# Performance work log

Hardware: AMD Instinct MI355X
Metric: run time of the kernel (lower is better)

The kernel has to match this reference:

```python
import jax, jax.numpy as jnp
import numpy as np

B, L, F_OP, F_EU, D, H = 4, 512, 10, 2, 128, 128


def setup_inputs() -> dict:
    key = jax.random.key(0)
    ks = jax.random.split(key, 16)

    def lin_w(k, fin, fout):
        # kaiming-ish init, stored [in, out] so forward is x @ W + b
        return (jax.random.normal(k, (fin, fout), jnp.float32) * (1.0 / np.sqrt(fin)))

    return {
        "inputs": jax.random.normal(ks[0], (B, L, F_OP), jnp.float32),
        "coords": jax.random.normal(ks[1], (B, L, F_EU), jnp.float32),
        "targets": jax.random.normal(ks[2], (B, L, 1), jnp.float32),
        "cc": jax.random.normal(ks[3], (B, L, F_EU), jnp.float32),
        # all sequences fully occupied -> static shapes everywhere
        "input_lenths": jnp.full((B,), L, dtype=jnp.int32),
        "Wc": lin_w(ks[4], F_OP + F_EU, D), "bc": jnp.zeros((D,), jnp.float32),
        "Wcc": lin_w(ks[5], F_OP + F_EU, D), "bcc": jnp.zeros((D,), jnp.float32),
        "Wa": lin_w(ks[6], D, D), "ba": jnp.zeros((D,), jnp.float32),
        "Wb": lin_w(ks[7], D, D), "bb": jnp.zeros((D,), jnp.float32),
        # GraphSAGE layer 1 (SAGEConv: lin_l on mean-aggregated msgs w/ bias, lin_r on root, no bias)
        "W1l": lin_w(ks[8], D, H), "b1l": jnp.zeros((H,), jnp.float32),
        "W1r": lin_w(ks[9], D, H),
        # GraphSAGE layer 2 -> scalar output
        "W2l": lin_w(ks[10], H, 1), "b2l": jnp.zeros((1,), jnp.float32),
        "W2r": lin_w(ks[11], H, 1),
    }


def _forward(inputs, coords, targets, cc,
             Wc, bc, Wcc, bcc, Wa, ba, Wb, bb,
             W1l, b1l, W1r, W2l, b2l, W2r):
    b_, l_, _ = inputs.shape
    d = Wa.shape[0]
    scale = 1.0 / np.sqrt(d)

    inputs_c = inputs - inputs[:, 0:1, :]
    i_emb = jnp.concatenate([inputs, coords], axis=-1) @ Wc + bc      # [B,L,D]
    ic_emb = jnp.concatenate([inputs_c, cc], axis=-1) @ Wcc + bcc     # [B,L,D]

    a = i_emb @ Wa + ba
    bt = i_emb @ Wb + bb
    a_c = ic_emb @ Wa + ba
    b_c = ic_emb @ Wb + bb

    adj = jnp.einsum('bid,bjd->bij', a, bt) * scale       # [B,L,L]
    adj_c = jnp.einsum('bid,bjd->bij', a_c, b_c) * scale

    # full lengths -> softmax_mask all False; MSE over the full matrices
    diff = jnp.mean((adj - adj_c) ** 2)

    # eval mode, full lengths: adj_mat_inplace has -inf only on the diagonal,
    # so exactly one entry per row is invalid after topk(k=L); the surviving
    # edges are the top (L-1) entries of adj per row (the row minimum drops).
    _, top_idx = jax.lax.top_k(adj, l_)                   # [B,L,L] descending
    src_local = top_idx[:, :, : l_ - 1]                   # [B,L,L-1]

    offsets = (jnp.arange(b_, dtype=jnp.int32) * l_)[:, None, None]
    src = (src_local.astype(jnp.int32) + offsets).reshape(-1)          # edge sources
    tgt = jnp.broadcast_to(jnp.arange(l_, dtype=jnp.int32)[None, :, None] + offsets,
                           (b_, l_, l_ - 1)).reshape(-1)               # edge targets

    x = (i_emb - ic_emb).reshape(b_ * l_, d)              # node features [N,D]
    n_nodes = b_ * l_
    deg = jnp.float32(l_ - 1)                             # every node has L-1 in-edges

    def sage_conv(h, Wl, bl, Wr):
        agg = jax.ops.segment_sum(h[src], tgt, num_segments=n_nodes) / deg
        return agg @ Wl + bl + h @ Wr

    h1 = jax.nn.relu(sage_conv(x, W1l, b1l, W1r))         # [N,H]
    out = sage_conv(h1, W2l, b2l, W2r)                    # [N,1]

    out_head = out.reshape(b_, l_, 1)[:, 0]               # first node per sample [B,1]
    target_head = targets[:, 0]                           # [B,1]
    return out_head, diff, target_head


def reference(inputs, coords, targets, cc, input_lenths,
              Wc, bc, Wcc, bcc, Wa, ba, Wb, bb,
              W1l, b1l, W1r, W2l, b2l, W2r):
    # input_lenths are all == L (full sequences) so masks are static no-ops.
    return _forward(inputs, coords, targets, cc,
                    Wc, bc, Wcc, bcc, Wa, ba, Wb, bb,
                    W1l, b1l, W1r, W2l, b2l, W2r)
```

## Files before the change

kernel.cpp:

```cpp
#include <hip/hip_runtime.h>
#include <math.h>

#define BB 4
#define LL 512
#define NROW (BB*LL)
#define DD 128
#define DEG 511.0f
#define SCALE 0.08838834764831845f

typedef short bf16x8 __attribute__((ext_vector_type(8)));
typedef float f32x4 __attribute__((ext_vector_type(4)));

static __device__ __forceinline__ ushort f2bf(float f) {
  unsigned u = __float_as_uint(f);
  u = (u + 0x7fffu + ((u >> 16) & 1u)) >> 16;
  return (ushort)u;
}

__global__ __launch_bounds__(256) void k_front(
    const float* __restrict__ inputs, const float* __restrict__ coords,
    const float* __restrict__ cc,
    const float* __restrict__ Wc, const float* __restrict__ bc,
    const float* __restrict__ Wcc, const float* __restrict__ bcc,
    const float* __restrict__ Wa, const float* __restrict__ ba,
    const float* __restrict__ Wb, const float* __restrict__ bb,
    const float* __restrict__ W1l, const float* __restrict__ W1r,
    ushort* __restrict__ bfA, ushort* __restrict__ bfB,
    ushort* __restrict__ bfAc, ushort* __restrict__ bfBc,
    float* __restrict__ P, float* __restrict__ Q,
    float* __restrict__ xpart) {
  int bx = blockIdx.x, m = blockIdx.y;
  int t = threadIdx.x;
  int row0 = bx * 16;
  int b = bx >> 5;
  __shared__ float fin1[16][12], fin2[16][12];
  __shared__ float Es[16][132];
  __shared__ float cs[2][128];
  if (t < 192) {
    int r = t / 12, k = t % 12;
    int row = row0 + r;
    float v1, v2;
    if (k < 10) {
      float v = inputs[row*10 + k];
      v1 = v;
      v2 = v - inputs[(b*LL)*10 + k];
    } else {
      v1 = coords[row*2 + (k-10)];
      v2 = cc[row*2 + (k-10)];
    }
    fin1[r][k] = v1;
    fin2[r][k] = v2;
  }
  __syncthreads();
  for (int it = 0; it < 8; ++it) {
    int idx = t + it*256;
    int r = idx >> 7, d = idx & 127;
    float e;
    if (m == 0) {
      e = bc[d];
#pragma unroll
      for (int k = 0; k < 12; ++k) e += fin1[r][k] * Wc[k*DD + d];
    } else if (m == 1) {
      e = bcc[d];
#pragma unroll
      for (int k = 0; k < 12; ++k) e += fin2[r][k] * Wcc[k*DD + d];
    } else {
      float e1 = bc[d], e2 = bcc[d];
#pragma unroll
      for (int k = 0; k < 12; ++k) {
        e1 += fin1[r][k] * Wc[k*DD + d];
        e2 += fin2[r][k] * Wcc[k*DD + d];
      }
      e = e1 - e2;
    }
    Es[r][d] = e;
  }
  __syncthreads();
  if (m == 2) {
    int d = t & 127, h = t >> 7;
    float s = 0.f;
#pragma unroll
    for (int r = 0; r < 8; ++r) s += Es[h*8 + r][d];
    cs[h][d] = s;
    __syncthreads();
    if (h == 0) xpart[bx*DD + d] = cs[0][d] + cs[1][d];
  }
  const float* U = (m == 2) ? W1l : Wa;
  const float* V = (m == 2) ? W1r : Wb;
  int tx = t & 31, ty = t >> 5;
  int d0 = tx*4, r0 = ty*2;
  float aU0[4]={0,0,0,0}, aU1[4]={0,0,0,0}, aV0[4]={0,0,0,0}, aV1[4]={0,0,0,0};
#pragma unroll 4
  for (int k = 0; k < DD; ++k) {
    float4 u = *(const float4*)&U[k*DD + d0];
    float4 v = *(const float4*)&V[k*DD + d0];
    float e0 = Es[r0][k], e1 = Es[r0+1][k];
    aU0[0]+=e0*u.x; aU0[1]+=e0*u.y; aU0[2]+=e0*u.z; aU0[3]+=e0*u.w;
    aU1[0]+=e1*u.x; aU1[1]+=e1*u.y; aU1[2]+=e1*u.z; aU1[3]+=e1*u.w;
    aV0[0]+=e0*v.x; aV0[1]+=e0*v.y; aV0[2]+=e0*v.z; aV0[3]+=e0*v.w;
    aV1[0]+=e1*v.x; aV1[1]+=e1*v.y; aV1[2]+=e1*v.z; aV1[3]+=e1*v.w;
  }
  if (m < 2) {
    float4 bu = *(const float4*)&ba[d0];
    float4 bw = *(const float4*)&bb[d0];
    ushort* dU = (m == 0) ? bfA : bfAc;
    ushort* dV = (m == 0) ? bfB : bfBc;
    ushort4 o;
    o = make_ushort4(f2bf(aU0[0]+bu.x), f2bf(aU0[1]+bu.y), f2bf(aU0[2]+bu.z), f2bf(aU0[3]+bu.w));
    *(ushort4*)&dU[(row0+r0)*DD + d0] = o;
    o = make_ushort4(f2bf(aU1[0]+bu.x), f2bf(aU1[1]+bu.y), f2bf(aU1[2]+bu.z), f2bf(aU1[3]+bu.w));
    *(ushort4*)&dU[(row0+r0+1)*DD + d0] = o;
    o = make_ushort4(f2bf(aV0[0]+bw.x), f2bf(aV0[1]+bw.y), f2bf(aV0[2]+bw.z), f2bf(aV0[3]+bw.w));
    *(ushort4*)&dV[(row0+r0)*DD + d0] = o;
    o = make_ushort4(f2bf(aV1[0]+bw.x), f2bf(aV1[1]+bw.y), f2bf(aV1[2]+bw.z), f2bf(aV1[3]+bw.w));
    *(ushort4*)&dV[(row0+r0+1)*DD + d0] = o;
  } else {
    *(float4*)&P[(row0+r0)*DD + d0]   = make_float4(aU0[0],aU0[1],aU0[2],aU0[3]);
    *(float4*)&P[(row0+r0+1)*DD + d0] = make_float4(aU1[0],aU1[1],aU1[2],aU1[3]);
    *(float4*)&Q[(row0+r0)*DD + d0]   = make_float4(aV0[0],aV0[1],aV0[2],aV0[3]);
    *(float4*)&Q[(row0+r0+1)*DD + d0] = make_float4(aV1[0],aV1[1],aV1[2],aV1[3]);
  }
}

__global__ __launch_bounds__(256, 2) void k_adj(
    const ushort* __restrict__ bfA, const ushort* __restrict__ bfB,
    const ushort* __restrict__ bfAc, const ushort* __restrict__ bfBc,
    float* __restrict__ diffpart, float* __restrict__ minval, int* __restrict__ minidx) {
  __shared__ ushort As[64][136], Acs[64][136], Bs[64][136], Bcs[64][136];
  __shared__ float red[256];
  int t = threadIdx.x;
  int ix = blockIdx.x, jy = blockIdx.y, b = blockIdx.z;
  int i0 = b*LL + ix*64, j0 = b*LL + jy*64;
  for (int it = 0; it < 4; ++it) {
    int chunk = t + it*256;
    int row = chunk >> 4, c = chunk & 15;
    *(uint4*)&As[row][c*8]  = *(const uint4*)&bfA[(size_t)(i0+row)*DD + c*8];
    *(uint4*)&Acs[row][c*8] = *(const uint4*)&bfAc[(size_t)(i0+row)*DD + c*8];
    *(uint4*)&Bs[row][c*8]  = *(const uint4*)&bfB[(size_t)(j0+row)*DD + c*8];
    *(uint4*)&Bcs[row][c*8] = *(const uint4*)&bfBc[(size_t)(j0+row)*DD + c*8];
  }
  __syncthreads();
  int wave = t >> 6, lane = t & 63;
  int rA = wave*16 + (lane & 15);
  int koff = (lane >> 4) * 8;
  bf16x8 av[4], acv[4];
#pragma unroll
  for (int ks = 0; ks < 4; ++ks) {
    av[ks]  = *(const bf16x8*)&As[rA][ks*32 + koff];
    acv[ks] = *(const bf16x8*)&Acs[rA][ks*32 + koff];
  }
  f32x4 zf = {0.f, 0.f, 0.f, 0.f};
  f32x4 acc[4], accc[4];
#pragma unroll
  for (int jt = 0; jt < 4; ++jt) { acc[jt] = zf; accc[jt] = zf; }
#pragma unroll
  for (int ks = 0; ks < 4; ++ks) {
#pragma unroll
    for (int jt = 0; jt < 4; ++jt) {
      bf16x8 bv  = *(const bf16x8*)&Bs[jt*16 + (lane&15)][ks*32 + koff];
      bf16x8 bcv = *(const bf16x8*)&Bcs[jt*16 + (lane&15)][ks*32 + koff];
      acc[jt]  = __builtin_amdgcn_mfma_f32_16x16x32_bf16(av[ks],  bv,  acc[jt],  0,0,0);
      accc[jt] = __builtin_amdgcn_mfma_f32_16x16x32_bf16(acv[ks], bcv, accc[jt], 0,0,0);
    }
  }
  int g = lane >> 4, c = lane & 15;
  float sq = 0.f;
#pragma unroll
  for (int r = 0; r < 4; ++r) {
    float mn = INFINITY; int mi = -1;
#pragma unroll
    for (int jt = 0; jt < 4; ++jt) {
      float v  = acc[jt][r]  * SCALE;
      float vc = accc[jt][r] * SCALE;
      float d = v - vc;
      sq += d*d;
      int j = j0 + jt*16 + c;
      if (v < mn || (v == mn && j > mi)) { mn = v; mi = j; }
    }
#pragma unroll
    for (int msk = 1; msk < 16; msk <<= 1) {
      float ov = __shfl_xor(mn, msk);
      int   oi = __shfl_xor(mi, msk);
      if (ov < mn || (ov == mn && oi > mi)) { mn = ov; mi = oi; }
    }
    if (c == 0) {
      int gi = i0 + wave*16 + g*4 + r;
      minval[gi*8 + jy] = mn;
      minidx[gi*8 + jy] = mi;
    }
  }
  red[t] = sq;
  __syncthreads();
  for (int off = 128; off > 0; off >>= 1) {
    if (t < off) red[t] += red[t+off];
    __syncthreads();
  }
  if (t == 0) diffpart[(b*8 + jy)*8 + ix] = red[0];
}

__global__ __launch_bounds__(256) void k_mid(
    const float* __restrict__ diffpart, const float* __restrict__ minval,
    const int* __restrict__ minidx, const float* __restrict__ targets,
    const float* __restrict__ xpart, const float* __restrict__ W1l,
    int* __restrict__ amin, float* __restrict__ sb, float* __restrict__ out) {
  int bz = blockIdx.x, t = threadIdx.x;
  __shared__ float red[256];
  __shared__ float cs[2][128];
  __shared__ float xs[128];
  if (bz < 4) {
    if (bz == 0) {
      red[t] = diffpart[t];
      __syncthreads();
      for (int off = 128; off > 0; off >>= 1) {
        if (t < off) red[t] += red[t+off];
        __syncthreads();
      }
      if (t == 0) out[4] = red[0] / (float)((float)BB*LL*LL);
      if (t < 4) out[5+t] = targets[t*LL];
    }
    for (int it = 0; it < 2; ++it) {
      int row = bz*LL + it*256 + t;
      float mv = minval[row*8]; int mi = minidx[row*8];
#pragma unroll
      for (int ch = 1; ch < 8; ++ch) {
        float v = minval[row*8+ch]; int i2 = minidx[row*8+ch];
        if (v < mv || (v == mv && i2 > mi)) { mv = v; mi = i2; }
      }
      amin[row] = mi;
    }
  } else {
    int b = bz - 4;
    int d = t & 127, h = t >> 7;
    float s = 0.f;
    for (int i = 0; i < 16; ++i) s += xpart[(b*32 + h*16 + i)*DD + d];
    cs[h][d] = s;
    __syncthreads();
    if (h == 0) xs[d] = cs[0][d] + cs[1][d];
    __syncthreads();
    float acc2 = 0.f;
    for (int k = 0; k < 64; ++k) acc2 += xs[h*64 + k] * W1l[(h*64 + k)*DD + d];
    cs[h][d] = acc2;
    __syncthreads();
    if (h == 0) sb[b*DD + d] = cs[0][d] + cs[1][d];
  }
}

__global__ __launch_bounds__(256) void k_h1(
    const float* __restrict__ P, const float* __restrict__ Q,
    const float* __restrict__ sb, const float* __restrict__ b1l,
    const int* __restrict__ amin, float* __restrict__ h1,
    float* __restrict__ h1part) {
  int bx = blockIdx.x, t = threadIdx.x;
  int d = t & 127, h = t >> 7;
  int b = bx >> 4;
  float base = sb[b*DD + d] * (1.0f/DEG) + b1l[d];
  float ps = 0.f;
  for (int rr = 0; rr < 16; ++rr) {
    int i = bx*32 + h*16 + rr;
    int am = amin[i];
    float v = base - P[am*DD + d] * (1.0f/DEG) + Q[i*DD + d];
    v = fmaxf(v, 0.f);
    h1[i*DD + d] = v;
    ps += v;
  }
  __shared__ float cs[2][128];
  cs[h][d] = ps;
  __syncthreads();
  if (h == 0) h1part[bx*DD + d] = cs[0][d] + cs[1][d];
}

__global__ __launch_bounds__(128) void k_final(
    const float* __restrict__ h1, const float* __restrict__ h1part,
    const int* __restrict__ amin,
    const float* __restrict__ W2l, const float* __restrict__ b2l,
    const float* __restrict__ W2r, float* __restrict__ out) {
  int b = blockIdx.x, d = threadIdx.x;
  float s = 0.f;
#pragma unroll
  for (int p = 0; p < 16; ++p) s += h1part[(b*16 + p)*DD + d];
  int am = amin[b*LL];
  float agg = (s - h1[am*DD + d]) * (1.0f/DEG);
  float v = agg * W2l[d] + h1[(b*LL)*DD + d] * W2r[d];
  __shared__ float red[128];
  red[d] = v;
  __syncthreads();
  for (int off = 64; off > 0; off >>= 1) {
    if (d < off) red[d] += red[d+off];
    __syncthreads();
  }
  if (d == 0) out[b] = red[0] + b2l[0];
}

extern "C" void kernel_launch(void* const* d_in, const int* in_sizes, int n_in,
                              void* d_out, int out_size, void* d_ws, size_t ws_size,
                              hipStream_t stream) {
  const float* inputs  = (const float*)d_in[0];
  const float* coords  = (const float*)d_in[1];
  const float* targets = (const float*)d_in[2];
  const float* cc      = (const float*)d_in[3];
  const float* Wc  = (const float*)d_in[5];
  const float* bc  = (const float*)d_in[6];
  const float* Wcc = (const float*)d_in[7];
  const float* bcc = (const float*)d_in[8];
  const float* Wa  = (const float*)d_in[9];
  const float* ba  = (const float*)d_in[10];
  const float* Wb  = (const float*)d_in[11];
  const float* bb  = (const float*)d_in[12];
  const float* W1l = (const float*)d_in[13];
  const float* b1l = (const float*)d_in[14];
  const float* W1r = (const float*)d_in[15];
  const float* W2l = (const float*)d_in[16];
  const float* b2l = (const float*)d_in[17];
  const float* W2r = (const float*)d_in[18];
  float* out = (float*)d_out;

  float* ws = (float*)d_ws;
  float* P  = ws;
  float* Q  = ws + (size_t)NROW*DD;
  float* h1 = ws + (size_t)2*NROW*DD;
  ushort* bfA  = (ushort*)(ws + (size_t)3*NROW*DD);
  ushort* bfB  = bfA  + (size_t)NROW*DD;
  ushort* bfAc = bfB  + (size_t)NROW*DD;
  ushort* bfBc = bfAc + (size_t)NROW*DD;
  float* xpart    = ws + (size_t)5*NROW*DD;
  float* h1part   = xpart + 128*DD;
  float* sb       = h1part + 64*DD;
  float* diffpart = sb + 4*DD;
  float* minval   = diffpart + 256;
  int*   minidx   = (int*)(minval + (size_t)NROW*8);
  int*   amin     = minidx + (size_t)NROW*8;

  k_front<<<dim3(128, 3), 256, 0, stream>>>(inputs, coords, cc, Wc, bc, Wcc, bcc,
                                            Wa, ba, Wb, bb, W1l, W1r,
                                            bfA, bfB, bfAc, bfBc, P, Q, xpart);
  k_adj  <<<dim3(8, 8, 4), 256, 0, stream>>>(bfA, bfB, bfAc, bfBc, diffpart, minval, minidx);
  k_mid  <<<8, 256, 0, stream>>>(diffpart, minval, minidx, targets, xpart, W1l, amin, sb, out);
  k_h1   <<<64, 256, 0, stream>>>(P, Q, sb, b1l, amin, h1, h1part);
  k_final<<<4, 128, 0, stream>>>(h1, h1part, amin, W2l, b2l, W2r, out);
}
```

Measured before the change: 42.03 us.

## Fuse mid and final stages into preceding kernels via last-block atomic counters

Removes the k_mid and k_final launches. A last-block-done atomic counter now runs the argmin merge, diff reduction and sb computation at the tail of k_adj, and the final output reduction at the tail of k_h1, with the counters reset in k_front. Separately, k_adj loads its A fragments straight from global into registers instead of staging them in LDS, which cuts shared memory use, and k_h1 vector-loads its amin indices. The cost is that the tail work runs serially in a single block, and the fences and atomics add a little overhead.

Measured after the change: 90.68 us. 116% more time.

```diff
diff --git a/kernel.cpp b/kernel.cpp
--- a/kernel.cpp
+++ b/kernel.cpp
@@ -28,9 +28,10 @@
     ushort* __restrict__ bfA, ushort* __restrict__ bfB,
     ushort* __restrict__ bfAc, ushort* __restrict__ bfBc,
     float* __restrict__ P, float* __restrict__ Q,
-    float* __restrict__ xpart) {
+    float* __restrict__ xpart, unsigned* __restrict__ cnt) {
   int bx = blockIdx.x, m = blockIdx.y;
   int t = threadIdx.x;
+  if (m == 0 && bx == 0 && t < 2) cnt[t] = 0u;
   int row0 = bx * 16;
   int b = bx >> 5;
   __shared__ float fin1[16][12], fin2[16][12];
@@ -122,33 +123,38 @@
   }
 }
 
-__global__ __launch_bounds__(256, 2) void k_adj(
+__global__ __launch_bounds__(256) void k_adj(
     const ushort* __restrict__ bfA, const ushort* __restrict__ bfB,
     const ushort* __restrict__ bfAc, const ushort* __restrict__ bfBc,
-    float* __restrict__ diffpart, float* __restrict__ minval, int* __restrict__ minidx) {
-  __shared__ ushort As[64][136], Acs[64][136], Bs[64][136], Bcs[64][136];
+    float* __restrict__ diffpart, float* __restrict__ minval, int* __restrict__ minidx,
+    const float* __restrict__ targets, const float* __restrict__ xpart,
+    const float* __restrict__ W1l,
+    int* __restrict__ amin, float* __restrict__ sb, float* __restrict__ out,
+    unsigned* __restrict__ cnt) {
+  __shared__ ushort Bs[64][136], Bcs[64][136];
   __shared__ float red[256];
+  __shared__ float cs2[2][128];
+  __shared__ float xs[128];
+  __shared__ unsigned done_s;
   int t = threadIdx.x;
   int ix = blockIdx.x, jy = blockIdx.y, b = blockIdx.z;
   int i0 = b*LL + ix*64, j0 = b*LL + jy*64;
+  int wave = t >> 6, lane = t & 63;
+  int rowA = i0 + wave*16 + (lane & 15);
+  int koff = (lane >> 4) * 8;
+  bf16x8 av[4], acv[4];
+#pragma unroll
+  for (int ks = 0; ks < 4; ++ks) {
+    av[ks]  = *(const bf16x8*)&bfA[(size_t)rowA*DD + ks*32 + koff];
+    acv[ks] = *(const bf16x8*)&bfAc[(size_t)rowA*DD + ks*32 + koff];
+  }
   for (int it = 0; it < 4; ++it) {
     int chunk = t + it*256;
     int row = chunk >> 4, c = chunk & 15;
-    *(uint4*)&As[row][c*8]  = *(const uint4*)&bfA[(size_t)(i0+row)*DD + c*8];
-    *(uint4*)&Acs[row][c*8] = *(const uint4*)&bfAc[(size_t)(i0+row)*DD + c*8];
     *(uint4*)&Bs[row][c*8]  = *(const uint4*)&bfB[(size_t)(j0+row)*DD + c*8];
     *(uint4*)&Bcs[row][c*8] = *(const uint4*)&bfBc[(size_t)(j0+row)*DD + c*8];
   }
   __syncthreads();
-  int wave = t >> 6, lane = t & 63;
-  int rA = wave*16 + (lane & 15);
-  int koff = (lane >> 4) * 8;
-  bf16x8 av[4], acv[4];
-#pragma unroll
-  for (int ks = 0; ks < 4; ++ks) {
-    av[ks]  = *(const bf16x8*)&As[rA][ks*32 + koff];
-    acv[ks] = *(const bf16x8*)&Acs[rA][ks*32 + koff];
-  }
   f32x4 zf = {0.f, 0.f, 0.f, 0.f};
   f32x4 acc[4], accc[4];
 #pragma unroll
@@ -196,30 +202,13 @@
     __syncthreads();
   }
   if (t == 0) diffpart[(b*8 + jy)*8 + ix] = red[0];
-}
-
-__global__ __launch_bounds__(256) void k_mid(
-    const float* __restrict__ diffpart, const float* __restrict__ minval,
-    const int* __restrict__ minidx, const float* __restrict__ targets,
-    const float* __restrict__ xpart, const float* __restrict__ W1l,
-    int* __restrict__ amin, float* __restrict__ sb, float* __restrict__ out) {
-  int bz = blockIdx.x, t = threadIdx.x;
-  __shared__ float red[256];
-  __shared__ float cs[2][128];
-  __shared__ float xs[128];
-  if (bz < 4) {
-    if (bz == 0) {
-      red[t] = diffpart[t];
-      __syncthreads();
-      for (int off = 128; off > 0; off >>= 1) {
-        if (t < off) red[t] += red[t+off];
-        __syncthreads();
-      }
-      if (t == 0) out[4] = red[0] / (float)((float)BB*LL*LL);
-      if (t < 4) out[5+t] = targets[t*LL];
-    }
-    for (int it = 0; it < 2; ++it) {
-      int row = bz*LL + it*256 + t;
+
+  __threadfence();
+  if (t == 0) done_s = atomicAdd(cnt, 1u);
+  __syncthreads();
+  if (done_s == 255u) {
+    __threadfence();
+    for (int row = t; row < NROW; row += 256) {
       float mv = minval[row*8]; int mi = minidx[row*8];
 #pragma unroll
       for (int ch = 1; ch < 8; ++ch) {
@@ -228,20 +217,29 @@
       }
       amin[row] = mi;
     }
-  } else {
-    int b = bz - 4;
+    red[t] = diffpart[t];
+    __syncthreads();
+    for (int off = 128; off > 0; off >>= 1) {
+      if (t < off) red[t] += red[t+off];
+      __syncthreads();
+    }
+    if (t == 0) out[4] = red[0] / (float)((float)BB*LL*LL);
+    if (t < 4) out[5+t] = targets[t*LL];
     int d = t & 127, h = t >> 7;
-    float s = 0.f;
-    for (int i = 0; i < 16; ++i) s += xpart[(b*32 + h*16 + i)*DD + d];
-    cs[h][d] = s;
-    __syncthreads();
-    if (h == 0) xs[d] = cs[0][d] + cs[1][d];
-    __syncthreads();
-    float acc2 = 0.f;
-    for (int k = 0; k < 64; ++k) acc2 += xs[h*64 + k] * W1l[(h*64 + k)*DD + d];
-    cs[h][d] = acc2;
-    __syncthreads();
-    if (h == 0) sb[b*DD + d] = cs[0][d] + cs[1][d];
+    for (int b2 = 0; b2 < 4; ++b2) {
+      float s = 0.f;
+      for (int i = 0; i < 16; ++i) s += xpart[(b2*32 + h*16 + i)*DD + d];
+      cs2[h][d] = s;
+      __syncthreads();
+      if (h == 0) xs[d] = cs2[0][d] + cs2[1][d];
+      __syncthreads();
+      float acc2 = 0.f;
+      for (int k = 0; k < 64; ++k) acc2 += xs[h*64 + k] * W1l[(h*64 + k)*DD + d];
+      cs2[h][d] = acc2;
+      __syncthreads();
+      if (h == 0) sb[b2*DD + d] = cs2[0][d] + cs2[1][d];
+      __syncthreads();
+    }
   }
 }
 
@@ -249,46 +247,57 @@
     const float* __restrict__ P, const float* __restrict__ Q,
     const float* __restrict__ sb, const float* __restrict__ b1l,
     const int* __restrict__ amin, float* __restrict__ h1,
-    float* __restrict__ h1part) {
+    float* __restrict__ h1part,
+    const float* __restrict__ W2l, const float* __restrict__ b2l,
+    const float* __restrict__ W2r, float* __restrict__ out,
+    unsigned* __restrict__ cnt) {
   int bx = blockIdx.x, t = threadIdx.x;
   int d = t & 127, h = t >> 7;
   int b = bx >> 4;
+  __shared__ float cs[2][128];
+  __shared__ float redf[128];
+  __shared__ unsigned done_s;
   float base = sb[b*DD + d] * (1.0f/DEG) + b1l[d];
+  int4 am4[4];
+#pragma unroll
+  for (int q = 0; q < 4; ++q) am4[q] = *(const int4*)&amin[bx*32 + h*16 + q*4];
   float ps = 0.f;
+#pragma unroll 4
   for (int rr = 0; rr < 16; ++rr) {
     int i = bx*32 + h*16 + rr;
-    int am = amin[i];
+    int am = ((const int*)am4)[rr];
     float v = base - P[am*DD + d] * (1.0f/DEG) + Q[i*DD + d];
     v = fmaxf(v, 0.f);
     h1[i*DD + d] = v;
     ps += v;
   }
-  __shared__ float cs[2][128];
   cs[h][d] = ps;
   __syncthreads();
   if (h == 0) h1part[bx*DD + d] = cs[0][d] + cs[1][d];
-}
-
-__global__ __launch_bounds__(128) void k_final(
-    const float* __restrict__ h1, const float* __restrict__ h1part,
-    const int* __restrict__ amin,
-    const float* __restrict__ W2l, const float* __restrict__ b2l,
-    const float* __restrict__ W2r, float* __restrict__ out) {
-  int b = blockIdx.x, d = threadIdx.x;
-  float s = 0.f;
-#pragma unroll
-  for (int p = 0; p < 16; ++p) s += h1part[(b*16 + p)*DD + d];
-  int am = amin[b*LL];
-  float agg = (s - h1[am*DD + d]) * (1.0f/DEG);
-  float v = agg * W2l[d] + h1[(b*LL)*DD + d] * W2r[d];
-  __shared__ float red[128];
-  red[d] = v;
-  __syncthreads();
-  for (int off = 64; off > 0; off >>= 1) {
-    if (d < off) red[d] += red[d+off];
-    __syncthreads();
-  }
-  if (d == 0) out[b] = red[0] + b2l[0];
+
+  __threadfence();
+  if (t == 0) done_s = atomicAdd(cnt, 1u);
+  __syncthreads();
+  if (done_s == 63u) {
+    __threadfence();
+    for (int b2 = 0; b2 < 4; ++b2) {
+      if (t < 128) {
+        float s = 0.f;
+#pragma unroll
+        for (int p = 0; p < 16; ++p) s += h1part[(b2*16 + p)*DD + t];
+        int am = amin[b2*LL];
+        float agg = (s - h1[am*DD + t]) * (1.0f/DEG);
+        redf[t] = agg * W2l[t] + h1[(b2*LL)*DD + t] * W2r[t];
+      }
+      __syncthreads();
+      for (int off = 64; off > 0; off >>= 1) {
+        if (t < off) redf[t] += redf[t+off];
+        __syncthreads();
+      }
+      if (t == 0) out[b2] = redf[0] + b2l[0];
+      __syncthreads();
+    }
+  }
 }
 
 extern "C" void kernel_launch(void* const* d_in, const int* in_sizes, int n_in,
@@ -329,12 +338,13 @@
   float* minval   = diffpart + 256;
   int*   minidx   = (int*)(minval + (size_t)NROW*8);
   int*   amin     = minidx + (size_t)NROW*8;
+  unsigned* cnt   = (unsigned*)(amin + NROW);
 
   k_front<<<dim3(128, 3), 256, 0, stream>>>(inputs, coords, cc, Wc, bc, Wcc, bcc,
                                             Wa, ba, Wb, bb, W1l, W1r,
-                                            bfA, bfB, bfAc, bfBc, P, Q, xpart);
-  k_adj  <<<dim3(8, 8, 4), 256, 0, stream>>>(bfA, bfB, bfAc, bfBc, diffpart, minval, minidx);
-  k_mid  <<<8, 256, 0, stream>>>(diffpart, minval, minidx, targets, xpart, W1l, amin, sb, out);
-  k_h1   <<<64, 256, 0, stream>>>(P, Q, sb, b1l, amin, h1, h1part);
-  k_final<<<4, 128, 0, stream>>>(h1, h1part, amin, W2l, b2l, W2r, out);
-}
+                                            bfA, bfB, bfAc, bfBc, P, Q, xpart, cnt);
+  k_adj  <<<dim3(8, 8, 4), 256, 0, stream>>>(bfA, bfB, bfAc, bfBc, diffpart, minval, minidx,
+                                             targets, xpart, W1l, amin, sb, out, cnt);
+  k_h1   <<<64, 256, 0, stream>>>(P, Q, sb, b1l, amin, h1, h1part,
+                                  W2l, b2l, W2r, out, cnt + 1);
+}
```

## Fuse argmin reduction into adjacency kernel and merge tail kernels into one

Applied to the files above, without the earlier changes.

The adjacency kernel now gives each block a 32-row strip covering all columns, so it computes the full row argmin and writes amin directly. This removes the minval/minidx partial buffers and the separate mid-stage reduction. The k_mid, k_h1 and k_final kernels are merged into one 1024-thread tail kernel per batch, which sums the h1 column totals without storing h1 and recomputes only the two h1 rows it needs. The change cuts the launch count from five to three, but k_adj drops to 64 blocks that read B operands straight from global memory without LDS staging, so it exposes less parallelism and gets less reuse.

Result: slower. 60.65 us (+44.3%).

```diff
diff --git a/kernel.cpp b/kernel.cpp
--- a/kernel.cpp
+++ b/kernel.cpp
@@ -122,173 +122,168 @@
   }
 }
 
-__global__ __launch_bounds__(256, 2) void k_adj(
+__global__ __launch_bounds__(256) void k_adj(
     const ushort* __restrict__ bfA, const ushort* __restrict__ bfB,
     const ushort* __restrict__ bfAc, const ushort* __restrict__ bfBc,
-    float* __restrict__ diffpart, float* __restrict__ minval, int* __restrict__ minidx) {
-  __shared__ ushort As[64][136], Acs[64][136], Bs[64][136], Bcs[64][136];
-  __shared__ float red[256];
+    float* __restrict__ diffpart, int* __restrict__ amin) {
   int t = threadIdx.x;
-  int ix = blockIdx.x, jy = blockIdx.y, b = blockIdx.z;
-  int i0 = b*LL + ix*64, j0 = b*LL + jy*64;
-  for (int it = 0; it < 4; ++it) {
-    int chunk = t + it*256;
-    int row = chunk >> 4, c = chunk & 15;
-    *(uint4*)&As[row][c*8]  = *(const uint4*)&bfA[(size_t)(i0+row)*DD + c*8];
-    *(uint4*)&Acs[row][c*8] = *(const uint4*)&bfAc[(size_t)(i0+row)*DD + c*8];
-    *(uint4*)&Bs[row][c*8]  = *(const uint4*)&bfB[(size_t)(j0+row)*DD + c*8];
-    *(uint4*)&Bcs[row][c*8] = *(const uint4*)&bfBc[(size_t)(j0+row)*DD + c*8];
-  }
-  __syncthreads();
-  int wave = t >> 6, lane = t & 63;
-  int rA = wave*16 + (lane & 15);
+  int ix = blockIdx.x;
+  int b  = blockIdx.y;
+  int i0 = b*LL + ix*32;
+  int w = t >> 6, lane = t & 63;
+  int isub = w & 1, jh = w >> 1;
+  int rowA = i0 + isub*16 + (lane & 15);
   int koff = (lane >> 4) * 8;
   bf16x8 av[4], acv[4];
 #pragma unroll
   for (int ks = 0; ks < 4; ++ks) {
-    av[ks]  = *(const bf16x8*)&As[rA][ks*32 + koff];
-    acv[ks] = *(const bf16x8*)&Acs[rA][ks*32 + koff];
-  }
-  f32x4 zf = {0.f, 0.f, 0.f, 0.f};
-  f32x4 acc[4], accc[4];
-#pragma unroll
-  for (int jt = 0; jt < 4; ++jt) { acc[jt] = zf; accc[jt] = zf; }
-#pragma unroll
-  for (int ks = 0; ks < 4; ++ks) {
-#pragma unroll
-    for (int jt = 0; jt < 4; ++jt) {
-      bf16x8 bv  = *(const bf16x8*)&Bs[jt*16 + (lane&15)][ks*32 + koff];
-      bf16x8 bcv = *(const bf16x8*)&Bcs[jt*16 + (lane&15)][ks*32 + koff];
-      acc[jt]  = __builtin_amdgcn_mfma_f32_16x16x32_bf16(av[ks],  bv,  acc[jt],  0,0,0);
-      accc[jt] = __builtin_amdgcn_mfma_f32_16x16x32_bf16(acv[ks], bcv, accc[jt], 0,0,0);
-    }
-  }
-  int g = lane >> 4, c = lane & 15;
+    av[ks]  = *(const bf16x8*)&bfA[(size_t)rowA*DD + ks*32 + koff];
+    acv[ks] = *(const bf16x8*)&bfAc[(size_t)rowA*DD + ks*32 + koff];
+  }
+  float mn[4] = {INFINITY, INFINITY, INFINITY, INFINITY};
+  int   mi[4] = {-1,-1,-1,-1};
   float sq = 0.f;
+  int c = lane & 15, g = lane >> 4;
+  for (int jc = jh*4; jc < jh*4 + 4; ++jc) {
+    int j0 = b*LL + jc*64;
+    f32x4 zf = {0.f,0.f,0.f,0.f};
+    f32x4 acc[4], accc[4];
+#pragma unroll
+    for (int jt = 0; jt < 4; ++jt) { acc[jt] = zf; accc[jt] = zf; }
+#pragma unroll
+    for (int ks = 0; ks < 4; ++ks) {
+#pragma unroll
+      for (int jt = 0; jt < 4; ++jt) {
+        bf16x8 bv  = *(const bf16x8*)&bfB[(size_t)(j0 + jt*16 + c)*DD + ks*32 + koff];
+        bf16x8 bcv = *(const bf16x8*)&bfBc[(size_t)(j0 + jt*16 + c)*DD + ks*32 + koff];
+        acc[jt]  = __builtin_amdgcn_mfma_f32_16x16x32_bf16(av[ks],  bv,  acc[jt],  0,0,0);
+        accc[jt] = __builtin_amdgcn_mfma_f32_16x16x32_bf16(acv[ks], bcv, accc[jt], 0,0,0);
+      }
+    }
+#pragma unroll
+    for (int r = 0; r < 4; ++r) {
+#pragma unroll
+      for (int jt = 0; jt < 4; ++jt) {
+        float v  = acc[jt][r]  * SCALE;
+        float vc = accc[jt][r] * SCALE;
+        float d = v - vc;
+        sq += d*d;
+        int j = j0 + jt*16 + c;
+        if (v < mn[r] || (v == mn[r] && j > mi[r])) { mn[r] = v; mi[r] = j; }
+      }
+    }
+  }
 #pragma unroll
   for (int r = 0; r < 4; ++r) {
-    float mn = INFINITY; int mi = -1;
-#pragma unroll
-    for (int jt = 0; jt < 4; ++jt) {
-      float v  = acc[jt][r]  * SCALE;
-      float vc = accc[jt][r] * SCALE;
-      float d = v - vc;
-      sq += d*d;
-      int j = j0 + jt*16 + c;
-      if (v < mn || (v == mn && j > mi)) { mn = v; mi = j; }
-    }
 #pragma unroll
     for (int msk = 1; msk < 16; msk <<= 1) {
-      float ov = __shfl_xor(mn, msk);
-      int   oi = __shfl_xor(mi, msk);
-      if (ov < mn || (ov == mn && oi > mi)) { mn = ov; mi = oi; }
-    }
-    if (c == 0) {
-      int gi = i0 + wave*16 + g*4 + r;
-      minval[gi*8 + jy] = mn;
-      minidx[gi*8 + jy] = mi;
-    }
-  }
+      float ov = __shfl_xor(mn[r], msk);
+      int   oi = __shfl_xor(mi[r], msk);
+      if (ov < mn[r] || (ov == mn[r] && oi > mi[r])) { mn[r] = ov; mi[r] = oi; }
+    }
+  }
+  __shared__ float mnS[2][32];
+  __shared__ int   miS[2][32];
+  if (c == 0) {
+#pragma unroll
+    for (int r = 0; r < 4; ++r) {
+      int rr = isub*16 + g*4 + r;
+      mnS[jh][rr] = mn[r];
+      miS[jh][rr] = mi[r];
+    }
+  }
+  __shared__ float red[256];
   red[t] = sq;
   __syncthreads();
   for (int off = 128; off > 0; off >>= 1) {
     if (t < off) red[t] += red[t+off];
     __syncthreads();
   }
-  if (t == 0) diffpart[(b*8 + jy)*8 + ix] = red[0];
-}
-
-__global__ __launch_bounds__(256) void k_mid(
-    const float* __restrict__ diffpart, const float* __restrict__ minval,
-    const int* __restrict__ minidx, const float* __restrict__ targets,
+  if (t == 0) diffpart[b*16 + ix] = red[0];
+  if (t < 32) {
+    float v0 = mnS[0][t]; int j0_ = miS[0][t];
+    float v1 = mnS[1][t]; int j1_ = miS[1][t];
+    amin[i0 + t] = (v1 <= v0) ? j1_ : j0_;
+  }
+}
+
+__global__ __launch_bounds__(1024) void k_tail(
+    const float* __restrict__ P, const float* __restrict__ Q,
     const float* __restrict__ xpart, const float* __restrict__ W1l,
-    int* __restrict__ amin, float* __restrict__ sb, float* __restrict__ out) {
-  int bz = blockIdx.x, t = threadIdx.x;
-  __shared__ float red[256];
-  __shared__ float cs[2][128];
-  __shared__ float xs[128];
-  if (bz < 4) {
-    if (bz == 0) {
-      red[t] = diffpart[t];
-      __syncthreads();
-      for (int off = 128; off > 0; off >>= 1) {
-        if (t < off) red[t] += red[t+off];
-        __syncthreads();
-      }
-      if (t == 0) out[4] = red[0] / (float)((float)BB*LL*LL);
-      if (t < 4) out[5+t] = targets[t*LL];
-    }
-    for (int it = 0; it < 2; ++it) {
-      int row = bz*LL + it*256 + t;
-      float mv = minval[row*8]; int mi = minidx[row*8];
-#pragma unroll
-      for (int ch = 1; ch < 8; ++ch) {
-        float v = minval[row*8+ch]; int i2 = minidx[row*8+ch];
-        if (v < mv || (v == mv && i2 > mi)) { mv = v; mi = i2; }
-      }
-      amin[row] = mi;
-    }
-  } else {
-    int b = bz - 4;
-    int d = t & 127, h = t >> 7;
-    float s = 0.f;
-    for (int i = 0; i < 16; ++i) s += xpart[(b*32 + h*16 + i)*DD + d];
-    cs[h][d] = s;
-    __syncthreads();
-    if (h == 0) xs[d] = cs[0][d] + cs[1][d];
-    __syncthreads();
-    float acc2 = 0.f;
-    for (int k = 0; k < 64; ++k) acc2 += xs[h*64 + k] * W1l[(h*64 + k)*DD + d];
-    cs[h][d] = acc2;
-    __syncthreads();
-    if (h == 0) sb[b*DD + d] = cs[0][d] + cs[1][d];
-  }
-}
-
-__global__ __launch_bounds__(256) void k_h1(
-    const float* __restrict__ P, const float* __restrict__ Q,
-    const float* __restrict__ sb, const float* __restrict__ b1l,
-    const int* __restrict__ amin, float* __restrict__ h1,
-    float* __restrict__ h1part) {
-  int bx = blockIdx.x, t = threadIdx.x;
-  int d = t & 127, h = t >> 7;
-  int b = bx >> 4;
-  float base = sb[b*DD + d] * (1.0f/DEG) + b1l[d];
-  float ps = 0.f;
-  for (int rr = 0; rr < 16; ++rr) {
-    int i = bx*32 + h*16 + rr;
-    int am = amin[i];
-    float v = base - P[am*DD + d] * (1.0f/DEG) + Q[i*DD + d];
-    v = fmaxf(v, 0.f);
-    h1[i*DD + d] = v;
-    ps += v;
-  }
-  __shared__ float cs[2][128];
-  cs[h][d] = ps;
-  __syncthreads();
-  if (h == 0) h1part[bx*DD + d] = cs[0][d] + cs[1][d];
-}
-
-__global__ __launch_bounds__(128) void k_final(
-    const float* __restrict__ h1, const float* __restrict__ h1part,
-    const int* __restrict__ amin,
+    const float* __restrict__ b1l, const int* __restrict__ amin,
+    const float* __restrict__ diffpart, const float* __restrict__ targets,
     const float* __restrict__ W2l, const float* __restrict__ b2l,
     const float* __restrict__ W2r, float* __restrict__ out) {
-  int b = blockIdx.x, d = threadIdx.x;
+  int b = blockIdx.x, t = threadIdx.x;
+  int d = t & 127, h = t >> 7;
+  __shared__ float part[8][128];
+  __shared__ float xs[128];
+  __shared__ float sbv[128];
   float s = 0.f;
 #pragma unroll
-  for (int p = 0; p < 16; ++p) s += h1part[(b*16 + p)*DD + d];
-  int am = amin[b*LL];
-  float agg = (s - h1[am*DD + d]) * (1.0f/DEG);
-  float v = agg * W2l[d] + h1[(b*LL)*DD + d] * W2r[d];
-  __shared__ float red[128];
-  red[d] = v;
-  __syncthreads();
-  for (int off = 64; off > 0; off >>= 1) {
-    if (d < off) red[d] += red[d+off];
-    __syncthreads();
-  }
-  if (d == 0) out[b] = red[0] + b2l[0];
+  for (int i = h; i < 32; i += 8) s += xpart[(b*32 + i)*DD + d];
+  part[h][d] = s;
+  __syncthreads();
+  if (h == 0) {
+    float v = 0.f;
+#pragma unroll
+    for (int q = 0; q < 8; ++q) v += part[q][d];
+    xs[d] = v;
+  }
+  __syncthreads();
+  float acc = 0.f;
+#pragma unroll
+  for (int k = h*16; k < h*16 + 16; ++k) acc += xs[k] * W1l[k*DD + d];
+  part[h][d] = acc;
+  __syncthreads();
+  if (h == 0) {
+    float v = 0.f;
+#pragma unroll
+    for (int q = 0; q < 8; ++q) v += part[q][d];
+    sbv[d] = v;
+  }
+  __syncthreads();
+  float base = sbv[d] * (1.0f/DEG) + b1l[d];
+  float csum = 0.f;
+  int r0 = b*LL + h*64;
+#pragma unroll 4
+  for (int r = 0; r < 64; ++r) {
+    int i = r0 + r;
+    int am = amin[i];
+    float v = base - P[(size_t)am*DD + d] * (1.0f/DEG) + Q[(size_t)i*DD + d];
+    csum += fmaxf(v, 0.f);
+  }
+  part[h][d] = csum;
+  __syncthreads();
+  if (h == 0) {
+    float colsum = 0.f;
+#pragma unroll
+    for (int q = 0; q < 8; ++q) colsum += part[q][d];
+    int head = b*LL;
+    int amh = amin[head];
+    int am2 = amin[amh];
+    float h1head = fmaxf(base - P[(size_t)amh*DD + d]*(1.0f/DEG) + Q[(size_t)head*DD + d], 0.f);
+    float h1am   = fmaxf(base - P[(size_t)am2*DD + d]*(1.0f/DEG) + Q[(size_t)amh*DD + d], 0.f);
+    float agg = (colsum - h1am) * (1.0f/DEG);
+    part[0][d] = agg * W2l[d] + h1head * W2r[d];
+  }
+  __syncthreads();
+  if (t < 64) {
+    float v = part[0][t] + part[0][t + 64];
+#pragma unroll
+    for (int msk = 32; msk > 0; msk >>= 1) v += __shfl_down(v, msk);
+    if (t == 0) out[b] = v + b2l[0];
+  }
+  if (b == 0) {
+    if (t >= 128 && t < 192) {
+      int q = t - 128;
+      float v = diffpart[q];
+#pragma unroll
+      for (int msk = 32; msk > 0; msk >>= 1) v += __shfl_down(v, msk);
+      if (q == 0) out[4] = v / (float)((float)BB*LL*LL);
+    }
+    if (t >= 192 && t < 196) out[5 + (t-192)] = targets[(t-192)*LL];
+  }
 }
 
 extern "C" void kernel_launch(void* const* d_in, const int* in_sizes, int n_in,
@@ -317,24 +312,18 @@
   float* ws = (float*)d_ws;
   float* P  = ws;
   float* Q  = ws + (size_t)NROW*DD;
-  float* h1 = ws + (size_t)2*NROW*DD;
-  ushort* bfA  = (ushort*)(ws + (size_t)3*NROW*DD);
+  ushort* bfA  = (ushort*)(ws + (size_t)2*NROW*DD);
   ushort* bfB  = bfA  + (size_t)NROW*DD;
   ushort* bfAc = bfB  + (size_t)NROW*DD;
   ushort* bfBc = bfAc + (size_t)NROW*DD;
-  float* xpart    = ws + (size_t)5*NROW*DD;
-  float* h1part   = xpart + 128*DD;
-  float* sb       = h1part + 64*DD;
-  float* diffpart = sb + 4*DD;
-  float* minval   = diffpart + 256;
-  int*   minidx   = (int*)(minval + (size_t)NROW*8);
-  int*   amin     = minidx + (size_t)NROW*8;
+  float* xpart    = ws + (size_t)4*NROW*DD;
+  float* diffpart = xpart + 128*DD;
+  int*   amin     = (int*)(diffpart + 64);
 
   k_front<<<dim3(128, 3), 256, 0, stream>>>(inputs, coords, cc, Wc, bc, Wcc, bcc,
                                             Wa, ba, Wb, bb, W1l, W1r,
                                             bfA, bfB, bfAc, bfBc, P, Q, xpart);
-  k_adj  <<<dim3(8, 8, 4), 256, 0, stream>>>(bfA, bfB, bfAc, bfBc, diffpart, minval, minidx);
-  k_mid  <<<8, 256, 0, stream>>>(diffpart, minval, minidx, targets, xpart, W1l, amin, sb, out);
-  k_h1   <<<64, 256, 0, stream>>>(P, Q, sb, b1l, amin, h1, h1part);
-  k_final<<<4, 128, 0, stream>>>(h1, h1part, amin, W2l, b2l, W2r, out);
-}
+  k_adj  <<<dim3(16, 4), 256, 0, stream>>>(bfA, bfB, bfAc, bfBc, diffpart, amin);
+  k_tail <<<4, 1024, 0, stream>>>(P, Q, xpart, W1l, b1l, amin, diffpart, targets,
+                                  W2l, b2l, W2r, out);
+}
```
